# Optimization experiments

Hardware: AMD Instinct MI355X
Metric: run time of the kernel (lower is better)

Reference implementation:

```python
import jax, jax.numpy as jnp
import numpy as np

NUM_GROUPS = 32
NUM_HEADS = 8
EPS = 1e-6


def group_norm(x, gamma, beta):
    B, C, H, W = x.shape
    xg = x.reshape(B, NUM_GROUPS, C // NUM_GROUPS, H, W)
    mean = xg.mean(axis=(2, 3, 4), keepdims=True)
    var = xg.var(axis=(2, 3, 4), keepdims=True)
    xn = (xg - mean) * jax.lax.rsqrt(var + EPS)
    xn = xn.reshape(B, C, H, W)
    return xn * gamma[None, :, None, None] + beta[None, :, None, None]


def setup_inputs() -> dict:
    key = jax.random.key(0)
    ks = jax.random.split(key, 3)
    B, C, H, W = 8, 512, 32, 32
    x = jax.random.normal(ks[0], (B, C, H, W), dtype=jnp.float32)
    # xavier_uniform for conv1x1: fan_in=C, fan_out per weight
    lim_qkv = float(np.sqrt(6.0 / (C + 3 * C)))
    w_qkv = jax.random.uniform(ks[1], (3 * C, C), minval=-lim_qkv, maxval=lim_qkv, dtype=jnp.float32)
    b_qkv = jnp.zeros((3 * C,), dtype=jnp.float32)
    lim_p = float(np.sqrt(6.0 / (C + C)))
    w_proj = jax.random.uniform(ks[2], (C, C), minval=-lim_p, maxval=lim_p, dtype=jnp.float32)
    b_proj = jnp.zeros((C,), dtype=jnp.float32)
    gamma = jnp.ones((C,), dtype=jnp.float32)
    beta = jnp.zeros((C,), dtype=jnp.float32)
    return {"x": x, "gamma": gamma, "beta": beta, "w_qkv": w_qkv, "b_qkv": b_qkv,
            "w_proj": w_proj, "b_proj": b_proj}


def reference(x, gamma, beta, w_qkv, b_qkv, w_proj, b_proj):
    B, C, H, W = x.shape
    N = H * W
    hd = C // NUM_HEADS
    scale = hd ** -0.5

    x_norm = group_norm(x, gamma, beta)
    # conv1x1 == channel GEMM: (B,C,H,W) -> (B,3C,H,W)
    qkv = jnp.einsum('bchw,oc->bohw', x_norm, w_qkv) + b_qkv[None, :, None, None]
    qkv = qkv.reshape(B, 3, NUM_HEADS, hd, N).transpose(1, 0, 2, 4, 3)
    q, k, v = qkv[0], qkv[1], qkv[2]

    attn = jnp.einsum('bhnd,bhmd->bhnm', q, k) * scale
    attn = jax.nn.softmax(attn, axis=-1)
    out = jnp.einsum('bhnm,bhmd->bhnd', attn, v)

    out = out.transpose(0, 1, 3, 2).reshape(B, C, H, W)
    out = jnp.einsum('bchw,oc->bohw', out, w_proj) + b_proj[None, :, None, None]
    return x + out
```

## Files before the change

kernel.cpp:

```cpp
#include <hip/hip_runtime.h>

#define LOG2E 1.4426950408889634f

typedef short bf16x8 __attribute__((ext_vector_type(8)));
typedef short short4v __attribute__((ext_vector_type(4)));
typedef float f32x4 __attribute__((ext_vector_type(4)));
typedef _Float16 half4v __attribute__((ext_vector_type(4)));
typedef unsigned u32x4 __attribute__((ext_vector_type(4)));
typedef unsigned __attribute__((address_space(1))) u32g;
typedef unsigned __attribute__((address_space(3))) u32l;

#define MFMA16(a, b, c) __builtin_amdgcn_mfma_f32_16x16x32_bf16((a), (b), (c), 0, 0, 0)

__device__ __forceinline__ short f2bf(float f) {
  unsigned u = __builtin_bit_cast(unsigned, f);
  u += 0x7FFFu + ((u >> 16) & 1u);
  return (short)(u >> 16);
}

__device__ __forceinline__ unsigned cvtpk(float lo, float hi) {
  unsigned r;
  asm("v_cvt_pk_bf16_f32 %0, %1, %2" : "=v"(r) : "v"(lo), "v"(hi));
  return r;
}

__device__ __forceinline__ void g2l16(void* lds, const void* g) {
  __builtin_amdgcn_global_load_lds((u32g*)const_cast<void*>(g), (u32l*)lds, 16, 0, 0);
}

__global__ __launch_bounds__(256) void gn_kernel(const float* __restrict__ x,
                                                 const float* __restrict__ gamma,
                                                 const float* __restrict__ beta,
                                                 short* __restrict__ xn_t) {
  __shared__ _Float16 xs[16 * 1024];
  __shared__ float red[8];
  const int bg = blockIdx.x;
  const int b = bg >> 5, g = bg & 31;
  const int t = threadIdx.x;
  const float4* gx4 = (const float4*)(x + (size_t)(b * 512 + g * 16) * 1024);
  float s1 = 0.f, s2 = 0.f;
  for (int i = 0; i < 16; ++i) {
    float4 v = gx4[t + 256 * i];
    s1 += (v.x + v.y) + (v.z + v.w);
    s2 += (v.x * v.x + v.y * v.y) + (v.z * v.z + v.w * v.w);
    half4v pk = {(_Float16)v.x, (_Float16)v.y, (_Float16)v.z, (_Float16)v.w};
    *(half4v*)((char*)xs + i * 2048 + ((8 * t) ^ ((i & 7) << 4))) = pk;
  }
  for (int m = 1; m < 64; m <<= 1) {
    s1 += __shfl_xor(s1, m);
    s2 += __shfl_xor(s2, m);
  }
  if ((t & 63) == 0) {
    red[(t >> 6) * 2] = s1;
    red[(t >> 6) * 2 + 1] = s2;
  }
  __syncthreads();
  s1 = (red[0] + red[2]) + (red[4] + red[6]);
  s2 = (red[1] + red[3]) + (red[5] + red[7]);
  const float mean = s1 * (1.f / 16384.f);
  const float var = s2 * (1.f / 16384.f) - mean * mean;
  const float rstd = rsqrtf(var + 1e-6f);
  const int ci = t & 15;
  const float ga = gamma[g * 16 + ci] * rstd;
  const float be = beta[g * 16 + ci] - mean * ga;
  short* dst = xn_t + (size_t)b * 1024 * 512 + g * 16 + ci;
  const int sw = (ci & 7) << 4;
  for (int i = 0; i < 64; ++i) {
    int n = (t >> 4) + 16 * i;
    float v = (float)*(const _Float16*)((const char*)xs + ci * 2048 + ((2 * n) ^ sw));
    dst[(size_t)n * 512] = f2bf(fmaf(v, ga, be));
  }
}

__global__ __launch_bounds__(256) void f2bf2_kernel(const float* __restrict__ s1,
                                                    short* __restrict__ d1, int n1,
                                                    const float* __restrict__ s2,
                                                    short* __restrict__ d2) {
  int i = blockIdx.x * 256 + threadIdx.x;
  const float* s = (i < n1) ? s1 : s2;
  short* d = (i < n1) ? d1 : d2;
  int j = (i < n1) ? i : i - n1;
  float4 v = ((const float4*)s)[j];
  short4v o = {f2bf(v.x), f2bf(v.y), f2bf(v.z), f2bf(v.w)};
  *(short4v*)(d + (size_t)j * 4) = o;
}

__global__ __launch_bounds__(256) void qkv_gemm(const short* __restrict__ W,
                                                const short* __restrict__ xn,
                                                const float* __restrict__ bias,
                                                short* __restrict__ qbuf,
                                                short* __restrict__ kbuf,
                                                short* __restrict__ vtbuf) {
  __shared__ short a_sm[3][128 * 32];
  __shared__ short b_sm[3][128 * 32];
  const int t = threadIdx.x;
  const int lane = t & 63, w = t >> 6;
  const int nbase = blockIdx.x * 128;
  const int mbase = blockIdx.y * 128;
  const int b = blockIdx.z;
  const short* Asrc = W + (size_t)mbase * 512;
  const short* Bsrc = xn + (size_t)b * 1024 * 512 + (size_t)nbase * 512;

  const int j0 = t, j1 = t + 256;
  const int r0 = j0 >> 2, c0 = ((j0 & 3) ^ ((j0 >> 3) & 3)) * 8;
  const int r1 = j1 >> 2, c1 = ((j1 & 3) ^ ((j1 >> 3) & 3)) * 8;

#define STAGE(bi, kt)                                                 \
  {                                                                   \
    const int k0s = (kt) * 32;                                        \
    g2l16(&a_sm[bi][j0 * 8], Asrc + (size_t)r0 * 512 + k0s + c0);     \
    g2l16(&a_sm[bi][j1 * 8], Asrc + (size_t)r1 * 512 + k0s + c1);     \
    g2l16(&b_sm[bi][j0 * 8], Bsrc + (size_t)r0 * 512 + k0s + c0);     \
    g2l16(&b_sm[bi][j1 * 8], Bsrc + (size_t)r1 * 512 + k0s + c1);     \
  }

  const int wm = (w >> 1) * 64, wn = (w & 1) * 64;
  const int col = lane & 15, rg = lane >> 4;

  f32x4 acc[4][4] = {};

  STAGE(0, 0)
  STAGE(1, 1)

  for (int kt = 0; kt < 16; ++kt) {
    const int cur = kt % 3;
    if (kt < 14) {
      STAGE((kt + 2) % 3, kt + 2)
      asm volatile("s_waitcnt vmcnt(8)" ::: "memory");
    } else if (kt == 14) {
      asm volatile("s_waitcnt vmcnt(4)" ::: "memory");
    } else {
      asm volatile("s_waitcnt vmcnt(0)" ::: "memory");
    }
    __builtin_amdgcn_s_barrier();
    __builtin_amdgcn_sched_barrier(0);

    bf16x8 af[4], bfr[4];
#pragma unroll
    for (int mf = 0; mf < 4; ++mf) {
      const int row = wm + mf * 16 + col;
      af[mf] = *(const bf16x8*)&a_sm[cur][row * 32 + ((rg ^ ((row >> 1) & 3)) * 8)];
    }
#pragma unroll
    for (int nf = 0; nf < 4; ++nf) {
      const int row = wn + nf * 16 + col;
      bfr[nf] = *(const bf16x8*)&b_sm[cur][row * 32 + ((rg ^ ((row >> 1) & 3)) * 8)];
    }
    __builtin_amdgcn_s_setprio(1);
#pragma unroll
    for (int mf = 0; mf < 4; ++mf)
#pragma unroll
      for (int nf = 0; nf < 4; ++nf)
        acc[mf][nf] = MFMA16(af[mf], bfr[nf], acc[mf][nf]);
    __builtin_amdgcn_s_setprio(0);
  }
#undef STAGE

  const int section = mbase >> 9;
  for (int mf = 0; mf < 4; ++mf) {
    const int o0 = mbase + wm + mf * 16 + rg * 4;
    const int h = (o0 >> 6) & 7, d0 = o0 & 63;
    float b4[4];
    for (int r = 0; r < 4; ++r) b4[r] = bias[o0 + r];
    for (int nf = 0; nf < 4; ++nf) {
      const int n = nbase + wn + nf * 16 + col;
      if (section < 2) {
        short4v pkv;
        for (int r = 0; r < 4; ++r) pkv[r] = f2bf(acc[mf][nf][r] + b4[r]);
        short* dst = (section == 0) ? qbuf : kbuf;
        *(short4v*)&dst[((size_t)(b * 8 + h) * 1024 + n) * 64 + d0] = pkv;
      } else {
        for (int r = 0; r < 4; ++r)
          vtbuf[((size_t)(b * 8 + h) * 64 + d0 + r) * 1024 + n] =
              f2bf(acc[mf][nf][r] + b4[r]);
      }
    }
  }
}

__global__ __launch_bounds__(512, 4) void attn_kernel(const short* __restrict__ qbuf,
                                                      const short* __restrict__ kbuf,
                                                      const short* __restrict__ vtbuf,
                                                      short* __restrict__ ao) {
  __shared__ char smem[65536];
  const int t = threadIdx.x, lane = t & 63, w = t >> 6;
  const int col = lane & 15, rg = lane >> 4;
  const int grp = w >> 2, wq = w & 3;
  const int tg = t & 255;
  const int bh = blockIdx.x, qt = blockIdx.y;
  const int b = bh >> 3, h = bh & 7;
  const int qbase = qt * 128 + wq * 32;

  short* kb_ = (short*)(smem + grp * 32768);
  short* vb_ = (short*)(smem + grp * 32768 + 16384);

  bf16x8 aq[2][2];
  {
    const short* qp = qbuf + ((size_t)bh * 1024 + qbase) * 64;
#pragma unroll
    for (int mf = 0; mf < 2; ++mf)
#pragma unroll
      for (int kc = 0; kc < 2; ++kc)
        aq[mf][kc] = *(const bf16x8*)&qp[(mf * 16 + col) * 64 + kc * 32 + rg * 8];
  }

  const short* kp0 = kbuf + (size_t)bh * 65536 + grp * 32768;
  const short* vp0 = vtbuf + (size_t)bh * 65536 + grp * 512;

  uint4 kr[2], vr[2];
#define LOADK(kt)                                                                  \
  _Pragma("unroll") for (int i = 0; i < 2; ++i) {                                  \
    int j = tg + 256 * i;                                                          \
    kr[i] = *(const uint4*)&kp0[((size_t)(kt)*64 + (j >> 3)) * 64 + (j & 7) * 8];  \
  }
#define LOADV(kt)                                                                  \
  _Pragma("unroll") for (int i = 0; i < 2; ++i) {                                  \
    int j = tg + 256 * i;                                                          \
    vr[i] = *(const uint4*)&vp0[(size_t)(j >> 3) * 1024 + (kt)*64 + (j & 7) * 8];  \
  }
#define WRITEK(bi)                                                                 \
  _Pragma("unroll") for (int i = 0; i < 2; ++i) {                                  \
    int j = tg + 256 * i;                                                          \
    int row = j >> 3, off = j & 7;                                                 \
    *(uint4*)((char*)kb_ + (bi)*8192 + row * 128 + ((off * 16) ^ ((row & 7) << 4))) = kr[i]; \
  }
#define WRITEV(bi)                                                                 \
  _Pragma("unroll") for (int i = 0; i < 2; ++i) {                                  \
    int j = tg + 256 * i;                                                          \
    int d = j >> 3, g = j & 7;                                                     \
    int base = (g >> 2) * 64 + (g & 1) * 32 + ((g >> 1) & 1) * 8;                  \
    char* vb = (char*)vb_ + (bi)*8192 + d * 128;                                   \
    uint2 lo = {vr[i].x, vr[i].y}, hi = {vr[i].z, vr[i].w};                        \
    *(uint2*)(vb + ((base) ^ ((d & 7) << 4))) = lo;                                \
    *(uint2*)(vb + ((base + 16) ^ ((d & 7) << 4))) = hi;                           \
  }

  f32x4 oacc[2][4] = {};
  float mrun[2] = {-3e38f, -3e38f}, lrun[2] = {0.f, 0.f};
  const float kSL2E = 0.125f * LOG2E;
  int cur = 0;

  LOADK(0) LOADV(0) WRITEK(0) WRITEV(0)
  __syncthreads();

  for (int kt = 0; kt < 8; ++kt) {
    if (kt < 7) { LOADK(kt + 1) LOADV(kt + 1) }

    f32x4 sT[2][4];
    __builtin_amdgcn_s_setprio(1);
#pragma unroll
    for (int nf = 0; nf < 4; ++nf) {
      const int n = nf * 16 + col;
      const char* kb = (const char*)kb_ + cur * 8192 + n * 128;
      const int sw = (n & 7) << 4;
      bf16x8 bk0 = *(const bf16x8*)(kb + ((rg * 16) ^ sw));
      bf16x8 bk1 = *(const bf16x8*)(kb + ((64 + rg * 16) ^ sw));
#pragma unroll
      for (int mf = 0; mf < 2; ++mf) {
        f32x4 z = {};
        z = MFMA16(bk0, aq[mf][0], z);
        sT[mf][nf] = MFMA16(bk1, aq[mf][1], z);
      }
    }
    __builtin_amdgcn_s_setprio(0);

    unsigned pk[2][4][2];
#pragma unroll
    for (int mf = 0; mf < 2; ++mf) {
      f32x4 mv = sT[mf][0];
#pragma unroll
      for (int nf = 1; nf < 4; ++nf)
#pragma unroll
        for (int r = 0; r < 4; ++r) mv[r] = fmaxf(mv[r], sT[mf][nf][r]);
      float mx = fmaxf(fmaxf(mv[0], mv[1]), fmaxf(mv[2], mv[3]));
      if (!__all(mx * 0.125f <= mrun[mf] + 8.f)) {
        float mxr = fmaxf(mx, __shfl_xor(mx, 16));
        mxr = fmaxf(mxr, __shfl_xor(mxr, 32));
        const float pmax = mxr * 0.125f;
        const float mnew = fmaxf(mrun[mf], pmax);
        const float alpha = __builtin_amdgcn_exp2f((mrun[mf] - mnew) * LOG2E);
        mrun[mf] = mnew;
        lrun[mf] *= alpha;
#pragma unroll
        for (int df = 0; df < 4; ++df) oacc[mf][df] *= alpha;
      }
      const float nege = mrun[mf] * LOG2E;
      float psum = 0.f;
#pragma unroll
      for (int nf = 0; nf < 4; ++nf) {
        float p0 = __builtin_amdgcn_exp2f(fmaf(sT[mf][nf][0], kSL2E, -nege));
        float p1 = __builtin_amdgcn_exp2f(fmaf(sT[mf][nf][1], kSL2E, -nege));
        float p2 = __builtin_amdgcn_exp2f(fmaf(sT[mf][nf][2], kSL2E, -nege));
        float p3 = __builtin_amdgcn_exp2f(fmaf(sT[mf][nf][3], kSL2E, -nege));
        psum += (p0 + p1) + (p2 + p3);
        pk[mf][nf][0] = cvtpk(p0, p1);
        pk[mf][nf][1] = cvtpk(p2, p3);
      }
      lrun[mf] += psum;
    }

    __builtin_amdgcn_s_setprio(1);
#pragma unroll
    for (int kc = 0; kc < 2; ++kc) {
      bf16x8 pb[2];
#pragma unroll
      for (int mf = 0; mf < 2; ++mf) {
        u32x4 pbu = {pk[mf][2 * kc][0], pk[mf][2 * kc][1], pk[mf][2 * kc + 1][0],
                     pk[mf][2 * kc + 1][1]};
        pb[mf] = __builtin_bit_cast(bf16x8, pbu);
      }
#pragma unroll
      for (int df = 0; df < 4; ++df) {
        const int d = df * 16 + col;
        bf16x8 av = *(const bf16x8*)((const char*)vb_ + cur * 8192 + d * 128 +
                                     ((kc * 64 + rg * 16) ^ ((d & 7) << 4)));
#pragma unroll
        for (int mf = 0; mf < 2; ++mf) oacc[mf][df] = MFMA16(av, pb[mf], oacc[mf][df]);
      }
    }
    __builtin_amdgcn_s_setprio(0);

    if (kt < 7) { WRITEK(cur ^ 1) WRITEV(cur ^ 1) }
    __syncthreads();
    cur ^= 1;
  }

#pragma unroll
  for (int mf = 0; mf < 2; ++mf) {
    float l = lrun[mf];
    l += __shfl_xor(l, 16);
    l += __shfl_xor(l, 32);
    lrun[mf] = l;
  }

  f32x4* o_lds = (f32x4*)smem;
  float* ml_lds = (float*)(smem + 32768);
  if (grp == 1) {
#pragma unroll
    for (int mf = 0; mf < 2; ++mf) {
#pragma unroll
      for (int df = 0; df < 4; ++df)
        o_lds[(((wq * 2 + mf) * 4) + df) * 64 + lane] = oacc[mf][df];
      ml_lds[((wq * 2 + mf) * 64 + lane) * 2] = mrun[mf];
      ml_lds[((wq * 2 + mf) * 64 + lane) * 2 + 1] = lrun[mf];
    }
  }
  __syncthreads();
  if (grp == 0) {
#pragma unroll
    for (int mf = 0; mf < 2; ++mf) {
      const float m1 = ml_lds[((wq * 2 + mf) * 64 + lane) * 2];
      const float l1 = ml_lds[((wq * 2 + mf) * 64 + lane) * 2 + 1];
      const float m = fmaxf(mrun[mf], m1);
      const float a0 = __builtin_amdgcn_exp2f((mrun[mf] - m) * LOG2E);
      const float a1 = __builtin_amdgcn_exp2f((m1 - m) * LOG2E);
      const float rl = 1.f / (lrun[mf] * a0 + l1 * a1);
      const int q = qbase + mf * 16 + col;
      short* dst = ao + ((size_t)b * 1024 + q) * 512 + h * 64;
#pragma unroll
      for (int df = 0; df < 4; ++df) {
        f32x4 o1 = o_lds[(((wq * 2 + mf) * 4) + df) * 64 + lane];
        short4v pkv;
#pragma unroll
        for (int r = 0; r < 4; ++r)
          pkv[r] = f2bf((oacc[mf][df][r] * a0 + o1[r] * a1) * rl);
        *(short4v*)&dst[df * 16 + rg * 4] = pkv;
      }
    }
  }
#undef LOADK
#undef LOADV
#undef WRITEK
#undef WRITEV
}

__global__ __launch_bounds__(256) void proj_gemm(const short* __restrict__ W,
                                                 const short* __restrict__ ao,
                                                 const float* __restrict__ bias,
                                                 const float* __restrict__ x,
                                                 float* __restrict__ out) {
  __shared__ short a_sm[3][64 * 32];
  __shared__ short b_sm[3][128 * 32];
  const int t = threadIdx.x;
  const int lane = t & 63, w = t >> 6;
  const int nbase = blockIdx.x * 128;
  const int mbase = blockIdx.y * 64;
  const int b = blockIdx.z;
  const short* Asrc = W + (size_t)mbase * 512;
  const short* Bsrc = ao + (size_t)b * 1024 * 512 + (size_t)nbase * 512;

  const int j0 = t, j1 = t + 256;
  const int r0 = j0 >> 2, c0 = ((j0 & 3) ^ ((j0 >> 3) & 3)) * 8;
  const int r1 = j1 >> 2, c1 = ((j1 & 3) ^ ((j1 >> 3) & 3)) * 8;

#define STAGE(bi, kt)                                                 \
  {                                                                   \
    const int k0s = (kt) * 32;                                        \
    g2l16(&a_sm[bi][j0 * 8], Asrc + (size_t)r0 * 512 + k0s + c0);     \
    g2l16(&b_sm[bi][j0 * 8], Bsrc + (size_t)r0 * 512 + k0s + c0);     \
    g2l16(&b_sm[bi][j1 * 8], Bsrc + (size_t)r1 * 512 + k0s + c1);     \
  }

  const int wm = (w >> 1) * 32, wn = (w & 1) * 64;
  const int col = lane & 15, rg = lane >> 4;

  f32x4 acc[2][4] = {};

  STAGE(0, 0)
  STAGE(1, 1)

  for (int kt = 0; kt < 16; ++kt) {
    const int cur = kt % 3;
    if (kt < 14) {
      STAGE((kt + 2) % 3, kt + 2)
      asm volatile("s_waitcnt vmcnt(6)" ::: "memory");
    } else if (kt == 14) {
      asm volatile("s_waitcnt vmcnt(3)" ::: "memory");
    } else {
      asm volatile("s_waitcnt vmcnt(0)" ::: "memory");
    }
    __builtin_amdgcn_s_barrier();
    __builtin_amdgcn_sched_barrier(0);

    bf16x8 af[2], bfr[4];
#pragma unroll
    for (int mf = 0; mf < 2; ++mf) {
      const int row = wm + mf * 16 + col;
      af[mf] = *(const bf16x8*)&a_sm[cur][row * 32 + ((rg ^ ((row >> 1) & 3)) * 8)];
    }
#pragma unroll
    for (int nf = 0; nf < 4; ++nf) {
      const int row = wn + nf * 16 + col;
      bfr[nf] = *(const bf16x8*)&b_sm[cur][row * 32 + ((rg ^ ((row >> 1) & 3)) * 8)];
    }
    __builtin_amdgcn_s_setprio(1);
#pragma unroll
    for (int mf = 0; mf < 2; ++mf)
#pragma unroll
      for (int nf = 0; nf < 4; ++nf)
        acc[mf][nf] = MFMA16(af[mf], bfr[nf], acc[mf][nf]);
    __builtin_amdgcn_s_setprio(0);
  }
#undef STAGE

  for (int mf = 0; mf < 2; ++mf) {
    const int o0 = mbase + wm + mf * 16 + rg * 4;
    float b4[4];
    for (int r = 0; r < 4; ++r) b4[r] = bias[o0 + r];
    for (int nf = 0; nf < 4; ++nf) {
      const int n = nbase + wn + nf * 16 + col;
      for (int r = 0; r < 4; ++r) {
        size_t idx = ((size_t)b * 512 + o0 + r) * 1024 + n;
        out[idx] = x[idx] + acc[mf][nf][r] + b4[r];
      }
    }
  }
}

extern "C" void kernel_launch(void* const* d_in, const int* in_sizes, int n_in,
                              void* d_out, int out_size, void* d_ws, size_t ws_size,
                              hipStream_t stream) {
  const float* x = (const float*)d_in[0];
  const float* gamma = (const float*)d_in[1];
  const float* beta = (const float*)d_in[2];
  const float* w_qkv = (const float*)d_in[3];
  const float* b_qkv = (const float*)d_in[4];
  const float* w_proj = (const float*)d_in[5];
  const float* b_proj = (const float*)d_in[6];
  float* out = (float*)d_out;

  char* ws = (char*)d_ws;
  short* xn_t = (short*)(ws);
  short* wqkv_b = (short*)(ws + 8388608);
  short* wproj_b = (short*)(ws + 9961472);
  short* qbuf = (short*)(ws + 10485760);
  short* kbuf = (short*)(ws + 18874368);
  short* vtbuf = (short*)(ws + 27262976);
  short* aobuf = (short*)(ws + 35651584);

  gn_kernel<<<dim3(256), dim3(256), 0, stream>>>(x, gamma, beta, xn_t);
  f2bf2_kernel<<<dim3(1024), dim3(256), 0, stream>>>(w_qkv, wqkv_b, 196608, w_proj,
                                                     wproj_b);
  qkv_gemm<<<dim3(8, 12, 8), dim3(256), 0, stream>>>(wqkv_b, xn_t, b_qkv, qbuf, kbuf,
                                                     vtbuf);
  attn_kernel<<<dim3(64, 8), dim3(512), 0, stream>>>(qbuf, kbuf, vtbuf, aobuf);
  proj_gemm<<<dim3(8, 8, 8), dim3(256), 0, stream>>>(wproj_b, aobuf, b_proj, x, out);
}
```

Measured before the change: 81.49 us.

## Use 512-thread QKV GEMM blocks and issue prefetch after barrier

The QKV GEMM block doubles from 4 to 8 waves, each computing a 64x32 sub-tile instead of 64x64. Each thread now issues one async LDS load per operand per stage. In both GEMMs the next-stage prefetch moves after the barrier, with the waitcnt lowered so only the current stage must have arrived. This aims to raise latency hiding through more waves, and to make the triple-buffer reuse safe without the old deeper vmcnt. The cost is fewer MFMAs per wave for each LDS fragment read, and higher register pressure under the (512,6) launch bound.

```diff
diff --git a/kernel.cpp b/kernel.cpp
--- a/kernel.cpp
+++ b/kernel.cpp
@@ -85,12 +85,12 @@
   *(short4v*)(d + (size_t)j * 4) = o;
 }
 
-__global__ __launch_bounds__(256) void qkv_gemm(const short* __restrict__ W,
-                                                const short* __restrict__ xn,
-                                                const float* __restrict__ bias,
-                                                short* __restrict__ qbuf,
-                                                short* __restrict__ kbuf,
-                                                short* __restrict__ vtbuf) {
+__global__ __launch_bounds__(512, 6) void qkv_gemm(const short* __restrict__ W,
+                                                   const short* __restrict__ xn,
+                                                   const float* __restrict__ bias,
+                                                   short* __restrict__ qbuf,
+                                                   short* __restrict__ kbuf,
+                                                   short* __restrict__ vtbuf) {
   __shared__ short a_sm[3][128 * 32];
   __shared__ short b_sm[3][128 * 32];
   const int t = threadIdx.x;
@@ -101,48 +101,43 @@
   const short* Asrc = W + (size_t)mbase * 512;
   const short* Bsrc = xn + (size_t)b * 1024 * 512 + (size_t)nbase * 512;
 
-  const int j0 = t, j1 = t + 256;
-  const int r0 = j0 >> 2, c0 = ((j0 & 3) ^ ((j0 >> 3) & 3)) * 8;
-  const int r1 = j1 >> 2, c1 = ((j1 & 3) ^ ((j1 >> 3) & 3)) * 8;
-
-#define STAGE(bi, kt)                                                 \
-  {                                                                   \
-    const int k0s = (kt) * 32;                                        \
-    g2l16(&a_sm[bi][j0 * 8], Asrc + (size_t)r0 * 512 + k0s + c0);     \
-    g2l16(&a_sm[bi][j1 * 8], Asrc + (size_t)r1 * 512 + k0s + c1);     \
-    g2l16(&b_sm[bi][j0 * 8], Bsrc + (size_t)r0 * 512 + k0s + c0);     \
-    g2l16(&b_sm[bi][j1 * 8], Bsrc + (size_t)r1 * 512 + k0s + c1);     \
-  }
-
-  const int wm = (w >> 1) * 64, wn = (w & 1) * 64;
+  const int j = t;
+  const int r = j >> 2, c = ((j & 3) ^ ((j >> 3) & 3)) * 8;
+
+#define STAGE(bi, kt)                                              \
+  {                                                                \
+    const int k0s = (kt) * 32;                                     \
+    g2l16(&a_sm[bi][j * 8], Asrc + (size_t)r * 512 + k0s + c);     \
+    g2l16(&b_sm[bi][j * 8], Bsrc + (size_t)r * 512 + k0s + c);     \
+  }
+
+  const int wm = (w >> 2) * 64, wn = (w & 3) * 32;
   const int col = lane & 15, rg = lane >> 4;
 
-  f32x4 acc[4][4] = {};
+  f32x4 acc[4][2] = {};
 
   STAGE(0, 0)
   STAGE(1, 1)
 
   for (int kt = 0; kt < 16; ++kt) {
     const int cur = kt % 3;
-    if (kt < 14) {
-      STAGE((kt + 2) % 3, kt + 2)
-      asm volatile("s_waitcnt vmcnt(8)" ::: "memory");
-    } else if (kt == 14) {
-      asm volatile("s_waitcnt vmcnt(4)" ::: "memory");
+    if (kt < 15) {
+      asm volatile("s_waitcnt vmcnt(2)" ::: "memory");
     } else {
       asm volatile("s_waitcnt vmcnt(0)" ::: "memory");
     }
     __builtin_amdgcn_s_barrier();
     __builtin_amdgcn_sched_barrier(0);
-
-    bf16x8 af[4], bfr[4];
+    if (kt < 14) STAGE((kt + 2) % 3, kt + 2)
+
+    bf16x8 af[4], bfr[2];
 #pragma unroll
     for (int mf = 0; mf < 4; ++mf) {
       const int row = wm + mf * 16 + col;
       af[mf] = *(const bf16x8*)&a_sm[cur][row * 32 + ((rg ^ ((row >> 1) & 3)) * 8)];
     }
 #pragma unroll
-    for (int nf = 0; nf < 4; ++nf) {
+    for (int nf = 0; nf < 2; ++nf) {
       const int row = wn + nf * 16 + col;
       bfr[nf] = *(const bf16x8*)&b_sm[cur][row * 32 + ((rg ^ ((row >> 1) & 3)) * 8)];
     }
@@ -150,7 +145,7 @@
 #pragma unroll
     for (int mf = 0; mf < 4; ++mf)
 #pragma unroll
-      for (int nf = 0; nf < 4; ++nf)
+      for (int nf = 0; nf < 2; ++nf)
         acc[mf][nf] = MFMA16(af[mf], bfr[nf], acc[mf][nf]);
     __builtin_amdgcn_s_setprio(0);
   }
@@ -161,18 +156,18 @@
     const int o0 = mbase + wm + mf * 16 + rg * 4;
     const int h = (o0 >> 6) & 7, d0 = o0 & 63;
     float b4[4];
-    for (int r = 0; r < 4; ++r) b4[r] = bias[o0 + r];
-    for (int nf = 0; nf < 4; ++nf) {
+    for (int r2 = 0; r2 < 4; ++r2) b4[r2] = bias[o0 + r2];
+    for (int nf = 0; nf < 2; ++nf) {
       const int n = nbase + wn + nf * 16 + col;
       if (section < 2) {
         short4v pkv;
-        for (int r = 0; r < 4; ++r) pkv[r] = f2bf(acc[mf][nf][r] + b4[r]);
+        for (int r2 = 0; r2 < 4; ++r2) pkv[r2] = f2bf(acc[mf][nf][r2] + b4[r2]);
         short* dst = (section == 0) ? qbuf : kbuf;
         *(short4v*)&dst[((size_t)(b * 8 + h) * 1024 + n) * 64 + d0] = pkv;
       } else {
-        for (int r = 0; r < 4; ++r)
-          vtbuf[((size_t)(b * 8 + h) * 64 + d0 + r) * 1024 + n] =
-              f2bf(acc[mf][nf][r] + b4[r]);
+        for (int r2 = 0; r2 < 4; ++r2)
+          vtbuf[((size_t)(b * 8 + h) * 64 + d0 + r2) * 1024 + n] =
+              f2bf(acc[mf][nf][r2] + b4[r2]);
       }
     }
   }
@@ -411,16 +406,14 @@
 
   for (int kt = 0; kt < 16; ++kt) {
     const int cur = kt % 3;
-    if (kt < 14) {
-      STAGE((kt + 2) % 3, kt + 2)
-      asm volatile("s_waitcnt vmcnt(6)" ::: "memory");
-    } else if (kt == 14) {
+    if (kt < 15) {
       asm volatile("s_waitcnt vmcnt(3)" ::: "memory");
     } else {
       asm volatile("s_waitcnt vmcnt(0)" ::: "memory");
     }
     __builtin_amdgcn_s_barrier();
     __builtin_amdgcn_sched_barrier(0);
+    if (kt < 14) STAGE((kt + 2) % 3, kt + 2)
 
     bf16x8 af[2], bfr[4];
 #pragma unroll
@@ -481,7 +474,7 @@
   gn_kernel<<<dim3(256), dim3(256), 0, stream>>>(x, gamma, beta, xn_t);
   f2bf2_kernel<<<dim3(1024), dim3(256), 0, stream>>>(w_qkv, wqkv_b, 196608, w_proj,
                                                      wproj_b);
-  qkv_gemm<<<dim3(8, 12, 8), dim3(256), 0, stream>>>(wqkv_b, xn_t, b_qkv, qbuf, kbuf,
+  qkv_gemm<<<dim3(8, 12, 8), dim3(512), 0, stream>>>(wqkv_b, xn_t, b_qkv, qbuf, kbuf,
                                                      vtbuf);
   attn_kernel<<<dim3(64, 8), dim3(512), 0, stream>>>(qbuf, kbuf, vtbuf, aobuf);
   proj_gemm<<<dim3(8, 8, 8), dim3(256), 0, stream>>>(wproj_b, aobuf, b_proj, x, out);
```

New measurement: 75.91 us. 6.8% less time.
